# Optimization experiments

Measured on AMD Instinct MI355X. Metric: run time of the kernel, lower is better.

The kernel has to match this reference:

```python
import jax, jax.numpy as jnp
import numpy as np

TOP_K = 2
ROUTE_SCALE = 1.0
EPS = 1e-20

B, S, D = 2, 512, 1024
E = 8            # num_experts
F = 768          # moe_intermediate_size
FS = 768 * 1     # shared expert intermediate (moe_intermediate_size * num_shared_experts)


def setup_inputs() -> dict:
    key = jax.random.key(0)
    ks = jax.random.split(key, 9)
    s = 0.02
    return {
        "hidden_states": jax.random.normal(ks[0], (B, S, D), dtype=jnp.float32),
        "W_gate_router": jax.random.normal(ks[1], (D, E), dtype=jnp.float32) * s,
        "expert_bias": jnp.zeros((E,), dtype=jnp.float32),
        "Wg": jax.random.normal(ks[2], (E, D, F), dtype=jnp.float32) * s,
        "Wu": jax.random.normal(ks[3], (E, D, F), dtype=jnp.float32) * s,
        "Wd": jax.random.normal(ks[4], (E, F, D), dtype=jnp.float32) * s,
        "Wg_s": jax.random.normal(ks[5], (D, FS), dtype=jnp.float32) * s,
        "Wu_s": jax.random.normal(ks[6], (D, FS), dtype=jnp.float32) * s,
        "Wd_s": jax.random.normal(ks[7], (FS, D), dtype=jnp.float32) * s,
    }


def reference(hidden_states, W_gate_router, expert_bias, Wg, Wu, Wd, Wg_s, Wu_s, Wd_s):
    b, s, d = hidden_states.shape
    x = hidden_states.reshape(-1, d)                      # [T, D]
    T = x.shape[0]

    # ---- token-choice top-k router (sigmoid scoring, route_norm) ----
    logits = x @ W_gate_router                            # [T, E]
    scores = jax.nn.sigmoid(logits.astype(jnp.float32))   # [T, E] fp32
    _, sel = jax.lax.top_k(scores + expert_bias, TOP_K)   # [T, K] (bias only for selection)
    top_scores = jnp.take_along_axis(scores, sel, axis=1)  # [T, K]
    top_scores = top_scores / (top_scores.sum(-1, keepdims=True) + EPS)  # route_norm
    top_scores = top_scores * ROUTE_SCALE

    # ---- shared expert (always active) ----
    shared = (jax.nn.silu(x @ Wg_s) * (x @ Wu_s)) @ Wd_s  # [T, D]

    # ---- dispatch: N = T*K routed slots (scatter-add is order-independent,
    #      so the torch stable-argsort grouping is mathematically a no-op) ----
    tok = jnp.repeat(jnp.arange(T), TOP_K)                # [N] source token per slot
    exp = sel.reshape(-1)                                 # [N] expert per slot
    w = top_scores.reshape(-1)                            # [N]
    xr = x[tok]                                           # [N, D]

    # per-expert SiLU-GLU MLP, vectorized over experts then select own expert's row
    h = jax.nn.silu(jnp.einsum('nd,edf->enf', xr, Wg)) * jnp.einsum('nd,edf->enf', xr, Wu)
    out_all = jnp.einsum('enf,efd->end', h, Wd)           # [E, N, D]
    routed = out_all[exp, jnp.arange(exp.shape[0])]       # [N, D]
    routed = (routed.astype(jnp.float32) * w[:, None]).astype(hidden_states.dtype)

    # ---- combine: scatter-add routed outputs onto shared output ----
    out = shared.at[tok].add(routed)                      # [T, D]
    return out.reshape(b, s, d)
```

## Files before the change

### kernel.cpp

```cpp
#include <hip/hip_runtime.h>
#include <hip/hip_bf16.h>
#include <math.h>

#define T_TOK   1024
#define D_DIM   1024
#define E_NUM   8
#define F_DIM   768
#define N_SLOTS 2048

typedef unsigned short u16;
typedef unsigned int   u32;
typedef __attribute__((ext_vector_type(8))) short bf16x8;
typedef __attribute__((ext_vector_type(4))) float f32x4;

#define WS_SEL    0
#define WS_WTS    8192
#define WS_BUCKET 16384
#define WS_COUNTS 49152
#define WS_OFFS   49216
#define WS_POS    49280
#define WS_XB     65536
#define WS_H      (WS_XB + 2097152)
#define WS_Y      (WS_H + 4718592)

__device__ __forceinline__ u16 f2bf(float x) {
    u32 u = __float_as_uint(x);
    u += 0x7fffu + ((u >> 16) & 1u);
    return (u16)(u >> 16);
}
#define PKBF(hi, lo) __builtin_amdgcn_perm(__float_as_uint(hi), __float_as_uint(lo), 0x07060302u)

__global__ __launch_bounds__(256) void xrouter_kernel(
    const float* __restrict__ X, const float* __restrict__ Wr,
    const float* __restrict__ bias, u16* __restrict__ Xb,
    int* __restrict__ sel, float* __restrict__ wts)
{
    int t = blockIdx.x * 4 + (threadIdx.x >> 6);
    int lane = threadIdx.x & 63;
    const float* xrow = X + (size_t)t * D_DIM;
    u16* brow = Xb + (size_t)t * D_DIM;
    float acc[E_NUM];
#pragma unroll
    for (int e = 0; e < E_NUM; ++e) acc[e] = 0.f;
#pragma unroll
    for (int q = 0; q < 4; ++q) {
        int d = q * 256 + lane * 4;
        float4 v = *(const float4*)(xrow + d);
        ushort4 o;
        o.x = f2bf(v.x); o.y = f2bf(v.y); o.z = f2bf(v.z); o.w = f2bf(v.w);
        *(ushort4*)(brow + d) = o;
        const float xv[4] = {v.x, v.y, v.z, v.w};
#pragma unroll
        for (int jj = 0; jj < 4; ++jj) {
            const float4* wr = (const float4*)(Wr + (size_t)(d + jj) * E_NUM);
            float4 w0 = wr[0], w1 = wr[1];
            acc[0] += xv[jj] * w0.x; acc[1] += xv[jj] * w0.y;
            acc[2] += xv[jj] * w0.z; acc[3] += xv[jj] * w0.w;
            acc[4] += xv[jj] * w1.x; acc[5] += xv[jj] * w1.y;
            acc[6] += xv[jj] * w1.z; acc[7] += xv[jj] * w1.w;
        }
    }
#pragma unroll
    for (int e = 0; e < E_NUM; ++e)
#pragma unroll
        for (int off = 32; off > 0; off >>= 1)
            acc[e] += __shfl_xor(acc[e], off);
    if (lane == 0) {
        float s[E_NUM], b[E_NUM];
#pragma unroll
        for (int e = 0; e < E_NUM; ++e) {
            s[e] = 1.f / (1.f + expf(-acc[e]));
            b[e] = s[e] + bias[e];
        }
        int i1 = 0; float b1 = b[0];
#pragma unroll
        for (int e = 1; e < E_NUM; ++e) if (b[e] > b1) { b1 = b[e]; i1 = e; }
        int i2 = -1; float b2 = -INFINITY;
#pragma unroll
        for (int e = 0; e < E_NUM; ++e) {
            if (e == i1) continue;
            if (b[e] > b2) { b2 = b[e]; i2 = e; }
        }
        float s1 = s[i1], s2 = s[i2];
        float denom = s1 + s2 + 1e-20f;
        sel[2 * t] = i1; sel[2 * t + 1] = i2;
        wts[2 * t] = s1 / denom; wts[2 * t + 1] = s2 / denom;
    }
}

__global__ __launch_bounds__(512) void dispatch_kernel(
    const int* __restrict__ sel, int* __restrict__ bucket,
    int* __restrict__ counts, int* __restrict__ offs, int* __restrict__ pos)
{
    __shared__ int soffs[E_NUM + 1];
    int e = threadIdx.x >> 6;
    int lane = threadIdx.x & 63;
    int running = 0;
    for (int base = 0; base < N_SLOTS; base += 64) {
        int slot = base + lane;
        bool mine = (sel[slot] == e);
        unsigned long long mask = __ballot(mine);
        if (mine) {
            int rank = running + __popcll(mask & ((1ull << lane) - 1ull));
            bucket[e * T_TOK + rank] = slot;
        }
        running += __popcll(mask);
    }
    if (lane == 0) counts[e] = running;
    __syncthreads();
    if (threadIdx.x == 0) {
        int o = 0;
        for (int k = 0; k < E_NUM; ++k) { soffs[k] = o; offs[k] = o; o += counts[k]; }
        soffs[E_NUM] = o; offs[E_NUM] = o;
    }
    __syncthreads();
    int base_off = soffs[e];
    for (int r = lane; r < running; r += 64)
        pos[bucket[e * T_TOK + r]] = base_off + r;
}

__global__ __launch_bounds__(256, 3) void proj1(
    const u16* __restrict__ Xb,
    const float* __restrict__ Wg, const float* __restrict__ Wu,
    const float* __restrict__ Wgs, const float* __restrict__ Wus,
    u16* __restrict__ H,
    const int* __restrict__ bucket, const int* __restrict__ counts, const int* __restrict__ offs)
{
    const int i = blockIdx.x;
    const int cxcd = i & 7, m = i >> 3;
    const int y = m & 31, phi = m >> 5;
    const int panel = phi * 8 + cxcd;
    if (panel >= 108) return;
    const int unit = panel / 12, x = panel - unit * 12;

    int nrows, rbase; const float *Bg, *Bu;
    if (unit < E_NUM) {
        nrows = counts[unit]; rbase = offs[unit];
        Bg = Wg + (size_t)unit * D_DIM * F_DIM;
        Bu = Wu + (size_t)unit * D_DIM * F_DIM;
    } else { nrows = T_TOK; rbase = N_SLOTS; Bg = Wgs; Bu = Wus; }
    const int row0 = y * 64;
    if (row0 >= nrows) return;

    __shared__ u16 smem[2][192 * 64];

    const int t = threadIdx.x;
    const int wv = t >> 6, lane = t & 63, l15 = lane & 15, g = lane >> 4;
    const int wm = wv >> 1, wn = wv & 1;

    const int ar = t >> 2, ac = t & 3;
    int grow = min(row0 + ar, nrows - 1);
    if (unit < E_NUM) grow = bucket[unit * T_TOK + grow] >> 1;
    const u16* srcA = Xb + (size_t)grow * D_DIM + ac * 8;
    const int wA0 = ar * 64 + ((ac     ^ (ar & 7)) * 8);
    const int wA1 = ar * 64 + (((ac+4) ^ (ar & 7)) * 8);

    const int bn = (t & 63) | (((t >> 6) & 1) << 6);
    const int bh = t >> 7;
    const float* srcB = ((bn < 64) ? Bg : Bu) + (size_t)(bh * 32) * F_DIM + x * 64 + (bn & 63);
    int wB[4];
#pragma unroll
    for (int q = 0; q < 4; ++q)
        wB[q] = (64 + bn) * 64 + (((bh * 4 + q) ^ (bn & 7)) * 8);

    f32x4 accg[2][2], accu[2][2];
    const f32x4 z4 = {0.f, 0.f, 0.f, 0.f};
#pragma unroll
    for (int ri = 0; ri < 2; ++ri)
#pragma unroll
        for (int ci = 0; ci < 2; ++ci) { accg[ri][ci] = z4; accu[ri][ci] = z4; }

    uint4 pa0, pa1;
    float pb[32];
#define LOAD1(kt) do { \
    pa0 = *(const uint4*)(srcA + (kt)); \
    pa1 = *(const uint4*)(srcA + (kt) + 32); \
    const float* _bp = srcB + (size_t)(kt) * F_DIM; \
    _Pragma("unroll") \
    for (int ii = 0; ii < 32; ++ii) pb[ii] = _bp[(size_t)ii * F_DIM]; \
} while (0)
#define WRITE1(buf) do { \
    *(uint4*)&smem[buf][wA0] = pa0; \
    *(uint4*)&smem[buf][wA1] = pa1; \
    _Pragma("unroll") \
    for (int q = 0; q < 4; ++q) { \
        u32 pk[4]; \
        _Pragma("unroll") \
        for (int j = 0; j < 4; ++j) pk[j] = PKBF(pb[8*q + 2*j + 1], pb[8*q + 2*j]); \
        *(uint4*)&smem[buf][wB[q]] = *(const uint4*)pk; \
    } \
} while (0)
#define COMP1(buf) do { \
    const u16* _p = smem[buf]; \
    _Pragma("unroll") \
    for (int kk = 0; kk < 2; ++kk) { \
        const int ch = (((kk << 2) | g) ^ (l15 & 7)) * 8; \
        bf16x8 _a[2], _bg[2], _bu[2]; \
        _Pragma("unroll") \
        for (int ri = 0; ri < 2; ++ri) \
            _a[ri] = *(const bf16x8*)&_p[(wm * 32 + ri * 16 + l15) * 64 + ch]; \
        _Pragma("unroll") \
        for (int ci = 0; ci < 2; ++ci) { \
            _bg[ci] = *(const bf16x8*)&_p[(64  + wn * 32 + ci * 16 + l15) * 64 + ch]; \
            _bu[ci] = *(const bf16x8*)&_p[(128 + wn * 32 + ci * 16 + l15) * 64 + ch]; \
        } \
        _Pragma("unroll") \
        for (int ri = 0; ri < 2; ++ri) \
            _Pragma("unroll") \
            for (int ci = 0; ci < 2; ++ci) { \
                accg[ri][ci] = __builtin_amdgcn_mfma_f32_16x16x32_bf16(_a[ri], _bg[ci], accg[ri][ci], 0, 0, 0); \
                accu[ri][ci] = __builtin_amdgcn_mfma_f32_16x16x32_bf16(_a[ri], _bu[ci], accu[ri][ci], 0, 0, 0); \
            } \
    } \
} while (0)

    LOAD1(0);
    for (int tt = 0; tt < 16; ++tt) {
        WRITE1(tt & 1);
        if (tt + 1 < 16) LOAD1((tt + 1) * 64);
        __syncthreads();
        COMP1(tt & 1);
    }
#undef LOAD1
#undef WRITE1
#undef COMP1

#pragma unroll
    for (int ri = 0; ri < 2; ++ri)
#pragma unroll
        for (int ci = 0; ci < 2; ++ci) {
            int n = x * 64 + wn * 32 + ci * 16 + l15;
#pragma unroll
            for (int r = 0; r < 4; ++r) {
                int row = row0 + wm * 32 + ri * 16 + g * 4 + r;
                if (row >= nrows) continue;
                float gv = accg[ri][ci][r];
                float uv = accu[ri][ci][r];
                H[(size_t)(rbase + row) * F_DIM + n] =
                    f2bf(gv / (1.f + __expf(-gv)) * uv);
            }
        }
}

__global__ __launch_bounds__(256, 3) void proj2(
    const u16* __restrict__ H,
    const float* __restrict__ Wd, const float* __restrict__ Wds,
    float* __restrict__ Y,
    const int* __restrict__ counts, const int* __restrict__ offs)
{
    const int i = blockIdx.x;
    const int cxcd = i & 7, m = i >> 3;
    const int y = m & 31, phi = m >> 5;
    const int panel = phi * 8 + cxcd;
    const int unit = panel >> 4, x = panel & 15;

    int nrows, rbase; const float* Bm;
    if (unit < E_NUM) {
        nrows = counts[unit]; rbase = offs[unit];
        Bm = Wd + (size_t)unit * F_DIM * D_DIM;
    } else { nrows = T_TOK; rbase = N_SLOTS; Bm = Wds; }
    const int row0 = y * 64;
    if (row0 >= nrows) return;

    __shared__ u16 smem[2][128 * 64];

    const int t = threadIdx.x;
    const int wv = t >> 6, lane = t & 63, l15 = lane & 15, g = lane >> 4;
    const int wm = wv >> 1, wn = wv & 1;

    const int ar = t >> 2, ac = t & 3;
    const int grow = rbase + min(row0 + ar, nrows - 1);
    const u16* srcA = H + (size_t)grow * F_DIM + ac * 8;
    const int wA0 = ar * 64 + ((ac     ^ (ar & 7)) * 8);
    const int wA1 = ar * 64 + (((ac+4) ^ (ar & 7)) * 8);

    const int bn = t & 63;
    const int bq = t >> 6;
    const float* srcB = Bm + (size_t)(bq * 16) * D_DIM + x * 64 + bn;
    int wB[2];
#pragma unroll
    for (int q = 0; q < 2; ++q)
        wB[q] = (64 + bn) * 64 + (((bq * 2 + q) ^ (bn & 7)) * 8);

    f32x4 acc[2][2];
    const f32x4 z4 = {0.f, 0.f, 0.f, 0.f};
#pragma unroll
    for (int ri = 0; ri < 2; ++ri)
#pragma unroll
        for (int ci = 0; ci < 2; ++ci) acc[ri][ci] = z4;

    uint4 pa0, pa1;
    float pb[16];
#define LOAD2(kt) do { \
    pa0 = *(const uint4*)(srcA + (kt)); \
    pa1 = *(const uint4*)(srcA + (kt) + 32); \
    const float* _bp = srcB + (size_t)(kt) * D_DIM; \
    _Pragma("unroll") \
    for (int ii = 0; ii < 16; ++ii) pb[ii] = _bp[(size_t)ii * D_DIM]; \
} while (0)
#define WRITE2(buf) do { \
    *(uint4*)&smem[buf][wA0] = pa0; \
    *(uint4*)&smem[buf][wA1] = pa1; \
    _Pragma("unroll") \
    for (int q = 0; q < 2; ++q) { \
        u32 pk[4]; \
        _Pragma("unroll") \
        for (int j = 0; j < 4; ++j) pk[j] = PKBF(pb[8*q + 2*j + 1], pb[8*q + 2*j]); \
        *(uint4*)&smem[buf][wB[q]] = *(const uint4*)pk; \
    } \
} while (0)
#define COMP2(buf) do { \
    const u16* _p = smem[buf]; \
    _Pragma("unroll") \
    for (int kk = 0; kk < 2; ++kk) { \
        const int ch = (((kk << 2) | g) ^ (l15 & 7)) * 8; \
        bf16x8 _a[2], _b[2]; \
        _Pragma("unroll") \
        for (int ri = 0; ri < 2; ++ri) \
            _a[ri] = *(const bf16x8*)&_p[(wm * 32 + ri * 16 + l15) * 64 + ch]; \
        _Pragma("unroll") \
        for (int ci = 0; ci < 2; ++ci) \
            _b[ci] = *(const bf16x8*)&_p[(64 + wn * 32 + ci * 16 + l15) * 64 + ch]; \
        _Pragma("unroll") \
        for (int ri = 0; ri < 2; ++ri) \
            _Pragma("unroll") \
            for (int ci = 0; ci < 2; ++ci) \
                acc[ri][ci] = __builtin_amdgcn_mfma_f32_16x16x32_bf16(_a[ri], _b[ci], acc[ri][ci], 0, 0, 0); \
    } \
} while (0)

    LOAD2(0);
    for (int tt = 0; tt < 12; ++tt) {
        WRITE2(tt & 1);
        if (tt + 1 < 12) LOAD2((tt + 1) * 64);
        __syncthreads();
        COMP2(tt & 1);
    }
#undef LOAD2
#undef WRITE2
#undef COMP2

#pragma unroll
    for (int ri = 0; ri < 2; ++ri)
#pragma unroll
        for (int ci = 0; ci < 2; ++ci) {
            int n = x * 64 + wn * 32 + ci * 16 + l15;
#pragma unroll
            for (int r = 0; r < 4; ++r) {
                int row = row0 + wm * 32 + ri * 16 + g * 4 + r;
                if (row >= nrows) continue;
                Y[(size_t)(rbase + row) * D_DIM + n] = acc[ri][ci][r];
            }
        }
}

__global__ __launch_bounds__(256) void combine_kernel(
    const float* __restrict__ Y, const int* __restrict__ pos,
    const float* __restrict__ wts, float* __restrict__ out)
{
    int t = blockIdx.x;
    int d = threadIdx.x * 4;
    int p0 = pos[2 * t], p1 = pos[2 * t + 1];
    float w0 = wts[2 * t], w1 = wts[2 * t + 1];
    float4 a = *(const float4*)(Y + (size_t)(N_SLOTS + t) * D_DIM + d);
    float4 b = *(const float4*)(Y + (size_t)p0 * D_DIM + d);
    float4 cc = *(const float4*)(Y + (size_t)p1 * D_DIM + d);
    float4 o;
    o.x = a.x + w0 * b.x + w1 * cc.x;
    o.y = a.y + w0 * b.y + w1 * cc.y;
    o.z = a.z + w0 * b.z + w1 * cc.z;
    o.w = a.w + w0 * b.w + w1 * cc.w;
    *(float4*)(out + (size_t)t * D_DIM + d) = o;
}

extern "C" void kernel_launch(void* const* d_in, const int* in_sizes, int n_in,
                              void* d_out, int out_size, void* d_ws, size_t ws_size,
                              hipStream_t stream) {
    const float* X    = (const float*)d_in[0];
    const float* Wr   = (const float*)d_in[1];
    const float* bias = (const float*)d_in[2];
    const float* Wg   = (const float*)d_in[3];
    const float* Wu   = (const float*)d_in[4];
    const float* Wd   = (const float*)d_in[5];
    const float* Wgs  = (const float*)d_in[6];
    const float* Wus  = (const float*)d_in[7];
    const float* Wds  = (const float*)d_in[8];
    float* out = (float*)d_out;

    char* ws = (char*)d_ws;
    int*   sel    = (int*)(ws + WS_SEL);
    float* wtsv   = (float*)(ws + WS_WTS);
    int*   bucket = (int*)(ws + WS_BUCKET);
    int*   counts = (int*)(ws + WS_COUNTS);
    int*   offs   = (int*)(ws + WS_OFFS);
    int*   pos    = (int*)(ws + WS_POS);
    u16*   Xb     = (u16*)(ws + WS_XB);
    u16*   H      = (u16*)(ws + WS_H);
    float* Y      = (float*)(ws + WS_Y);

    xrouter_kernel<<<256, 256, 0, stream>>>(X, Wr, bias, Xb, sel, wtsv);
    dispatch_kernel<<<1, 512, 0, stream>>>(sel, bucket, counts, offs, pos);

    proj1<<<3584, 256, 0, stream>>>(Xb, Wg, Wu, Wgs, Wus, H, bucket, counts, offs);
    proj2<<<4608, 256, 0, stream>>>(H, Wd, Wds, Y, counts, offs);
    combine_kernel<<<T_TOK, 256, 0, stream>>>(Y, pos, wtsv, out);
}
```

Baseline: 85.23 us.

## Use 128-row M tiles with 32-wide K steps in both MoE GEMMs

Both projection kernels now compute 128 rows per block instead of 64 and step K by 32 instead of 64. The LDS tile gets a new XOR swizzle, and the grid is halved. Each block now reuses every fp32 weight tile it loads and converts across twice as many rows, which roughly halves global weight traffic. The costs are more accumulator registers under a higher occupancy target of 4, twice as many barriers per block, and more wasted rows in partially filled expert buckets.

```diff
diff --git a/kernel.cpp b/kernel.cpp
--- a/kernel.cpp
+++ b/kernel.cpp
@@ -29,6 +29,10 @@
     return (u16)(u >> 16);
 }
 #define PKBF(hi, lo) __builtin_amdgcn_perm(__float_as_uint(hi), __float_as_uint(lo), 0x07060302u)
+
+__device__ __forceinline__ int phys(int r, int c) {
+    return r * 32 + ((c ^ ((r >> 1) & 3)) << 3);
+}
 
 __global__ __launch_bounds__(256) void xrouter_kernel(
     const float* __restrict__ X, const float* __restrict__ Wr,
@@ -119,7 +123,7 @@
         pos[bucket[e * T_TOK + r]] = base_off + r;
 }
 
-__global__ __launch_bounds__(256, 3) void proj1(
+__global__ __launch_bounds__(256, 4) void proj1(
     const u16* __restrict__ Xb,
     const float* __restrict__ Wg, const float* __restrict__ Wu,
     const float* __restrict__ Wgs, const float* __restrict__ Wus,
@@ -128,7 +132,7 @@
 {
     const int i = blockIdx.x;
     const int cxcd = i & 7, m = i >> 3;
-    const int y = m & 31, phi = m >> 5;
+    const int y = m & 15, phi = m >> 4;
     const int panel = phi * 8 + cxcd;
     if (panel >= 108) return;
     const int unit = panel / 12, x = panel - unit * 12;
@@ -139,85 +143,88 @@
         Bg = Wg + (size_t)unit * D_DIM * F_DIM;
         Bu = Wu + (size_t)unit * D_DIM * F_DIM;
     } else { nrows = T_TOK; rbase = N_SLOTS; Bg = Wgs; Bu = Wus; }
-    const int row0 = y * 64;
+    const int row0 = y * 128;
     if (row0 >= nrows) return;
 
-    __shared__ u16 smem[2][192 * 64];
+    __shared__ u16 smem[2][256 * 32];
 
     const int t = threadIdx.x;
     const int wv = t >> 6, lane = t & 63, l15 = lane & 15, g = lane >> 4;
     const int wm = wv >> 1, wn = wv & 1;
 
-    const int ar = t >> 2, ac = t & 3;
+    const int ar = t >> 1, ah = t & 1;
     int grow = min(row0 + ar, nrows - 1);
     if (unit < E_NUM) grow = bucket[unit * T_TOK + grow] >> 1;
-    const u16* srcA = Xb + (size_t)grow * D_DIM + ac * 8;
-    const int wA0 = ar * 64 + ((ac     ^ (ar & 7)) * 8);
-    const int wA1 = ar * 64 + (((ac+4) ^ (ar & 7)) * 8);
-
-    const int bn = (t & 63) | (((t >> 6) & 1) << 6);
-    const int bh = t >> 7;
-    const float* srcB = ((bn < 64) ? Bg : Bu) + (size_t)(bh * 32) * F_DIM + x * 64 + (bn & 63);
-    int wB[4];
-#pragma unroll
-    for (int q = 0; q < 4; ++q)
-        wB[q] = (64 + bn) * 64 + (((bh * 4 + q) ^ (bn & 7)) * 8);
-
-    f32x4 accg[2][2], accu[2][2];
+    const u16* srcA = Xb + (size_t)grow * D_DIM + ah * 16;
+    const int wA0 = phys(ar, 2 * ah);
+    const int wA1 = phys(ar, 2 * ah + 1);
+
+    const int bn = t & 127, kh2 = t >> 7;
+    const float* srcB = ((bn < 64) ? Bg : Bu) + (size_t)(kh2 * 16) * F_DIM + x * 64 + (bn & 63);
+    const int wB0 = phys(128 + bn, 2 * kh2);
+    const int wB1 = phys(128 + bn, 2 * kh2 + 1);
+
+    int offA[4], offG[2], offU[2];
+#pragma unroll
+    for (int ri = 0; ri < 4; ++ri)
+        offA[ri] = phys(wm * 64 + ri * 16 + l15, g);
+#pragma unroll
+    for (int ci = 0; ci < 2; ++ci) {
+        offG[ci] = phys(128 + wn * 32 + ci * 16 + l15, g);
+        offU[ci] = phys(192 + wn * 32 + ci * 16 + l15, g);
+    }
+
+    f32x4 accg[4][2], accu[4][2];
     const f32x4 z4 = {0.f, 0.f, 0.f, 0.f};
 #pragma unroll
-    for (int ri = 0; ri < 2; ++ri)
+    for (int ri = 0; ri < 4; ++ri)
 #pragma unroll
         for (int ci = 0; ci < 2; ++ci) { accg[ri][ci] = z4; accu[ri][ci] = z4; }
 
     uint4 pa0, pa1;
-    float pb[32];
+    float pb[16];
 #define LOAD1(kt) do { \
     pa0 = *(const uint4*)(srcA + (kt)); \
-    pa1 = *(const uint4*)(srcA + (kt) + 32); \
+    pa1 = *(const uint4*)(srcA + (kt) + 8); \
     const float* _bp = srcB + (size_t)(kt) * F_DIM; \
     _Pragma("unroll") \
-    for (int ii = 0; ii < 32; ++ii) pb[ii] = _bp[(size_t)ii * F_DIM]; \
+    for (int j = 0; j < 16; ++j) pb[j] = _bp[(size_t)j * F_DIM]; \
 } while (0)
 #define WRITE1(buf) do { \
     *(uint4*)&smem[buf][wA0] = pa0; \
     *(uint4*)&smem[buf][wA1] = pa1; \
-    _Pragma("unroll") \
-    for (int q = 0; q < 4; ++q) { \
-        u32 pk[4]; \
-        _Pragma("unroll") \
-        for (int j = 0; j < 4; ++j) pk[j] = PKBF(pb[8*q + 2*j + 1], pb[8*q + 2*j]); \
-        *(uint4*)&smem[buf][wB[q]] = *(const uint4*)pk; \
+    u32 pk0[4], pk1[4]; \
+    _Pragma("unroll") \
+    for (int j = 0; j < 4; ++j) { \
+        pk0[j] = PKBF(pb[2*j + 1], pb[2*j]); \
+        pk1[j] = PKBF(pb[8 + 2*j + 1], pb[8 + 2*j]); \
     } \
+    *(uint4*)&smem[buf][wB0] = *(const uint4*)pk0; \
+    *(uint4*)&smem[buf][wB1] = *(const uint4*)pk1; \
 } while (0)
 #define COMP1(buf) do { \
     const u16* _p = smem[buf]; \
-    _Pragma("unroll") \
-    for (int kk = 0; kk < 2; ++kk) { \
-        const int ch = (((kk << 2) | g) ^ (l15 & 7)) * 8; \
-        bf16x8 _a[2], _bg[2], _bu[2]; \
-        _Pragma("unroll") \
-        for (int ri = 0; ri < 2; ++ri) \
-            _a[ri] = *(const bf16x8*)&_p[(wm * 32 + ri * 16 + l15) * 64 + ch]; \
+    bf16x8 _a[4], _bg[2], _bu[2]; \
+    _Pragma("unroll") \
+    for (int ri = 0; ri < 4; ++ri) _a[ri] = *(const bf16x8*)&_p[offA[ri]]; \
+    _Pragma("unroll") \
+    for (int ci = 0; ci < 2; ++ci) { \
+        _bg[ci] = *(const bf16x8*)&_p[offG[ci]]; \
+        _bu[ci] = *(const bf16x8*)&_p[offU[ci]]; \
+    } \
+    _Pragma("unroll") \
+    for (int ri = 0; ri < 4; ++ri) \
         _Pragma("unroll") \
         for (int ci = 0; ci < 2; ++ci) { \
-            _bg[ci] = *(const bf16x8*)&_p[(64  + wn * 32 + ci * 16 + l15) * 64 + ch]; \
-            _bu[ci] = *(const bf16x8*)&_p[(128 + wn * 32 + ci * 16 + l15) * 64 + ch]; \
+            accg[ri][ci] = __builtin_amdgcn_mfma_f32_16x16x32_bf16(_a[ri], _bg[ci], accg[ri][ci], 0, 0, 0); \
+            accu[ri][ci] = __builtin_amdgcn_mfma_f32_16x16x32_bf16(_a[ri], _bu[ci], accu[ri][ci], 0, 0, 0); \
         } \
-        _Pragma("unroll") \
-        for (int ri = 0; ri < 2; ++ri) \
-            _Pragma("unroll") \
-            for (int ci = 0; ci < 2; ++ci) { \
-                accg[ri][ci] = __builtin_amdgcn_mfma_f32_16x16x32_bf16(_a[ri], _bg[ci], accg[ri][ci], 0, 0, 0); \
-                accu[ri][ci] = __builtin_amdgcn_mfma_f32_16x16x32_bf16(_a[ri], _bu[ci], accu[ri][ci], 0, 0, 0); \
-            } \
-    } \
 } while (0)
 
     LOAD1(0);
-    for (int tt = 0; tt < 16; ++tt) {
+    for (int tt = 0; tt < 32; ++tt) {
         WRITE1(tt & 1);
-        if (tt + 1 < 16) LOAD1((tt + 1) * 64);
+        if (tt + 1 < 32) LOAD1((tt + 1) * 32);
         __syncthreads();
         COMP1(tt & 1);
     }
@@ -226,13 +233,13 @@
 #undef COMP1
 
 #pragma unroll
-    for (int ri = 0; ri < 2; ++ri)
+    for (int ri = 0; ri < 4; ++ri)
 #pragma unroll
         for (int ci = 0; ci < 2; ++ci) {
             int n = x * 64 + wn * 32 + ci * 16 + l15;
 #pragma unroll
             for (int r = 0; r < 4; ++r) {
-                int row = row0 + wm * 32 + ri * 16 + g * 4 + r;
+                int row = row0 + wm * 64 + ri * 16 + g * 4 + r;
                 if (row >= nrows) continue;
                 float gv = accg[ri][ci][r];
                 float uv = accu[ri][ci][r];
@@ -242,7 +249,7 @@
         }
 }
 
-__global__ __launch_bounds__(256, 3) void proj2(
+__global__ __launch_bounds__(256, 4) void proj2(
     const u16* __restrict__ H,
     const float* __restrict__ Wd, const float* __restrict__ Wds,
     float* __restrict__ Y,
@@ -250,7 +257,7 @@
 {
     const int i = blockIdx.x;
     const int cxcd = i & 7, m = i >> 3;
-    const int y = m & 31, phi = m >> 5;
+    const int y = m & 15, phi = m >> 4;
     const int panel = phi * 8 + cxcd;
     const int unit = panel >> 4, x = panel & 15;
 
@@ -259,80 +266,75 @@
         nrows = counts[unit]; rbase = offs[unit];
         Bm = Wd + (size_t)unit * F_DIM * D_DIM;
     } else { nrows = T_TOK; rbase = N_SLOTS; Bm = Wds; }
-    const int row0 = y * 64;
+    const int row0 = y * 128;
     if (row0 >= nrows) return;
 
-    __shared__ u16 smem[2][128 * 64];
+    __shared__ u16 smem[2][192 * 32];
 
     const int t = threadIdx.x;
     const int wv = t >> 6, lane = t & 63, l15 = lane & 15, g = lane >> 4;
     const int wm = wv >> 1, wn = wv & 1;
 
-    const int ar = t >> 2, ac = t & 3;
+    const int ar = t >> 1, ah = t & 1;
     const int grow = rbase + min(row0 + ar, nrows - 1);
-    const u16* srcA = H + (size_t)grow * F_DIM + ac * 8;
-    const int wA0 = ar * 64 + ((ac     ^ (ar & 7)) * 8);
-    const int wA1 = ar * 64 + (((ac+4) ^ (ar & 7)) * 8);
-
-    const int bn = t & 63;
-    const int bq = t >> 6;
-    const float* srcB = Bm + (size_t)(bq * 16) * D_DIM + x * 64 + bn;
-    int wB[2];
-#pragma unroll
-    for (int q = 0; q < 2; ++q)
-        wB[q] = (64 + bn) * 64 + (((bq * 2 + q) ^ (bn & 7)) * 8);
-
-    f32x4 acc[2][2];
+    const u16* srcA = H + (size_t)grow * F_DIM + ah * 16;
+    const int wA0 = phys(ar, 2 * ah);
+    const int wA1 = phys(ar, 2 * ah + 1);
+
+    const int bn = t & 63, kq = t >> 6;
+    const float* srcB = Bm + (size_t)(kq * 8) * D_DIM + x * 64 + bn;
+    const int wB0 = phys(128 + bn, kq);
+
+    int offA[4], offB[2];
+#pragma unroll
+    for (int ri = 0; ri < 4; ++ri)
+        offA[ri] = phys(wm * 64 + ri * 16 + l15, g);
+#pragma unroll
+    for (int ci = 0; ci < 2; ++ci)
+        offB[ci] = phys(128 + wn * 32 + ci * 16 + l15, g);
+
+    f32x4 acc[4][2];
     const f32x4 z4 = {0.f, 0.f, 0.f, 0.f};
 #pragma unroll
-    for (int ri = 0; ri < 2; ++ri)
+    for (int ri = 0; ri < 4; ++ri)
 #pragma unroll
         for (int ci = 0; ci < 2; ++ci) acc[ri][ci] = z4;
 
     uint4 pa0, pa1;
-    float pb[16];
+    float pb[8];
 #define LOAD2(kt) do { \
     pa0 = *(const uint4*)(srcA + (kt)); \
-    pa1 = *(const uint4*)(srcA + (kt) + 32); \
+    pa1 = *(const uint4*)(srcA + (kt) + 8); \
     const float* _bp = srcB + (size_t)(kt) * D_DIM; \
     _Pragma("unroll") \
-    for (int ii = 0; ii < 16; ++ii) pb[ii] = _bp[(size_t)ii * D_DIM]; \
+    for (int j = 0; j < 8; ++j) pb[j] = _bp[(size_t)j * D_DIM]; \
 } while (0)
 #define WRITE2(buf) do { \
     *(uint4*)&smem[buf][wA0] = pa0; \
     *(uint4*)&smem[buf][wA1] = pa1; \
-    _Pragma("unroll") \
-    for (int q = 0; q < 2; ++q) { \
-        u32 pk[4]; \
-        _Pragma("unroll") \
-        for (int j = 0; j < 4; ++j) pk[j] = PKBF(pb[8*q + 2*j + 1], pb[8*q + 2*j]); \
-        *(uint4*)&smem[buf][wB[q]] = *(const uint4*)pk; \
-    } \
+    u32 pk[4]; \
+    _Pragma("unroll") \
+    for (int j = 0; j < 4; ++j) pk[j] = PKBF(pb[2*j + 1], pb[2*j]); \
+    *(uint4*)&smem[buf][wB0] = *(const uint4*)pk; \
 } while (0)
 #define COMP2(buf) do { \
     const u16* _p = smem[buf]; \
-    _Pragma("unroll") \
-    for (int kk = 0; kk < 2; ++kk) { \
-        const int ch = (((kk << 2) | g) ^ (l15 & 7)) * 8; \
-        bf16x8 _a[2], _b[2]; \
-        _Pragma("unroll") \
-        for (int ri = 0; ri < 2; ++ri) \
-            _a[ri] = *(const bf16x8*)&_p[(wm * 32 + ri * 16 + l15) * 64 + ch]; \
+    bf16x8 _a[4], _b[2]; \
+    _Pragma("unroll") \
+    for (int ri = 0; ri < 4; ++ri) _a[ri] = *(const bf16x8*)&_p[offA[ri]]; \
+    _Pragma("unroll") \
+    for (int ci = 0; ci < 2; ++ci) _b[ci] = *(const bf16x8*)&_p[offB[ci]]; \
+    _Pragma("unroll") \
+    for (int ri = 0; ri < 4; ++ri) \
         _Pragma("unroll") \
         for (int ci = 0; ci < 2; ++ci) \
-            _b[ci] = *(const bf16x8*)&_p[(64 + wn * 32 + ci * 16 + l15) * 64 + ch]; \
-        _Pragma("unroll") \
-        for (int ri = 0; ri < 2; ++ri) \
-            _Pragma("unroll") \
-            for (int ci = 0; ci < 2; ++ci) \
-                acc[ri][ci] = __builtin_amdgcn_mfma_f32_16x16x32_bf16(_a[ri], _b[ci], acc[ri][ci], 0, 0, 0); \
-    } \
+            acc[ri][ci] = __builtin_amdgcn_mfma_f32_16x16x32_bf16(_a[ri], _b[ci], acc[ri][ci], 0, 0, 0); \
 } while (0)
 
     LOAD2(0);
-    for (int tt = 0; tt < 12; ++tt) {
+    for (int tt = 0; tt < 24; ++tt) {
         WRITE2(tt & 1);
-        if (tt + 1 < 12) LOAD2((tt + 1) * 64);
+        if (tt + 1 < 24) LOAD2((tt + 1) * 32);
         __syncthreads();
         COMP2(tt & 1);
     }
@@ -341,13 +343,13 @@
 #undef COMP2
 
 #pragma unroll
-    for (int ri = 0; ri < 2; ++ri)
+    for (int ri = 0; ri < 4; ++ri)
 #pragma unroll
         for (int ci = 0; ci < 2; ++ci) {
             int n = x * 64 + wn * 32 + ci * 16 + l15;
 #pragma unroll
             for (int r = 0; r < 4; ++r) {
-                int row = row0 + wm * 32 + ri * 16 + g * 4 + r;
+                int row = row0 + wm * 64 + ri * 16 + g * 4 + r;
                 if (row >= nrows) continue;
                 Y[(size_t)(rbase + row) * D_DIM + n] = acc[ri][ci][r];
             }
@@ -401,7 +403,7 @@
     xrouter_kernel<<<256, 256, 0, stream>>>(X, Wr, bias, Xb, sel, wtsv);
     dispatch_kernel<<<1, 512, 0, stream>>>(sel, bucket, counts, offs, pos);
 
-    proj1<<<3584, 256, 0, stream>>>(Xb, Wg, Wu, Wgs, Wus, H, bucket, counts, offs);
-    proj2<<<4608, 256, 0, stream>>>(H, Wd, Wds, Y, counts, offs);
+    proj1<<<1792, 256, 0, stream>>>(Xb, Wg, Wu, Wgs, Wus, H, bucket, counts, offs);
+    proj2<<<2304, 256, 0, stream>>>(H, Wd, Wds, Y, counts, offs);
     combine_kernel<<<T_TOK, 256, 0, stream>>>(Y, pos, wtsv, out);
 }
```

New measurement: 115.7 us. 1.36x slower.
